# Kernel tuning notes

Hardware: AMD Instinct MI355X
Metric: run time of the kernel (lower is better)

Reference implementation:

```python
import jax, jax.numpy as jnp
import numpy as np

QUERY_DIM = 1024
CONTEXT_DIM = 768
HEADS = 16
DIM_HEAD = 64
INNER = HEADS * DIM_HEAD  # 1024
SCALE = DIM_HEAD ** -0.5


def setup_inputs() -> dict:
    key = jax.random.key(0)
    ks = jax.random.split(key, 8)
    b, nq, nkv = 4, 2048, 1024
    x = jax.random.normal(ks[0], (b, nq, QUERY_DIM), dtype=jnp.float32)
    context = jax.random.normal(ks[1], (b, nkv, CONTEXT_DIM), dtype=jnp.float32)
    mask = jax.random.randint(ks[2], (b, nkv), 0, 2).astype(jnp.bool_)
    s = 0.02
    Wq = jax.random.normal(ks[3], (QUERY_DIM, INNER), dtype=jnp.float32) * s
    Wk = jax.random.normal(ks[4], (CONTEXT_DIM, INNER), dtype=jnp.float32) * s
    Wv = jax.random.normal(ks[5], (CONTEXT_DIM, INNER), dtype=jnp.float32) * s
    Wo = jax.random.normal(ks[6], (INNER, QUERY_DIM), dtype=jnp.float32) * s
    bo = jnp.zeros((QUERY_DIM,), dtype=jnp.float32)
    return {"x": x, "context": context, "mask": mask,
            "Wq": Wq, "Wk": Wk, "Wv": Wv, "Wo": Wo, "bo": bo}


def reference(x, context, mask, Wq, Wk, Wv, Wo, bo):
    b, nq, _ = x.shape
    nkv = context.shape[1]
    h, d = HEADS, DIM_HEAD
    # QKV projections (no bias, as in nn.Linear(..., bias=False))
    q = (x @ Wq).reshape(b, nq, h, d).transpose(0, 2, 1, 3)       # [b,h,i,d]
    k = (context @ Wk).reshape(b, nkv, h, d).transpose(0, 2, 1, 3)  # [b,h,j,d]
    v = (context @ Wv).reshape(b, nkv, h, d).transpose(0, 2, 1, 3)  # [b,h,j,d]
    sim = jnp.einsum('bhid,bhjd->bhij', q, k) * SCALE
    # mask is per-key [b, j]; broadcast over heads and query positions
    neg = jnp.finfo(sim.dtype).min
    sim = jnp.where(mask[:, None, None, :], sim, neg)
    attn = jax.nn.softmax(sim, axis=-1)
    out = jnp.einsum('bhij,bhjd->bhid', attn, v)                  # [b,h,i,d]
    out = out.transpose(0, 2, 1, 3).reshape(b, nq, h * d)          # [b,i,hd]
    return out @ Wo + bo
```

## Files before the change

kernel.cpp:

```cpp
#include <hip/hip_runtime.h>

typedef unsigned short u16;
typedef __attribute__((ext_vector_type(8))) __bf16 bf16x8;
typedef __attribute__((ext_vector_type(4))) float f32x4;
typedef __attribute__((ext_vector_type(4))) u16 u16x4;

#define NB 4
#define NQ 2048
#define NKV 1024
#define NH 16
#define DH 64
#define DIN 1024
#define DCTX 768
#define ATT_SCALE 0.125f
#define NEGBIG -1e30f

__device__ inline u16 f2bf(float f) {
  unsigned u = __builtin_bit_cast(unsigned, f);
  u += 0x7FFFu + ((u >> 16) & 1u);
  return (u16)(u >> 16);
}

__device__ inline unsigned cvtpk(float lo, float hi) {
  unsigned r;
  asm("v_cvt_pk_bf16_f32 %0, %1, %2" : "=v"(r) : "v"(lo), "v"(hi));
  return r;
}

__global__ __launch_bounds__(256) void build_bias(const void* __restrict__ mask,
                                                  float* __restrict__ biasg) {
  __shared__ int notInt, notFloat;
  if (threadIdx.x == 0) { notInt = 0; notFloat = 0; }
  __syncthreads();
  const unsigned* mw = (const unsigned*)mask;
  int bad_i = 0, bad_f = 0;
#pragma unroll
  for (int e = 0; e < 4; e++) {
    unsigned v = mw[threadIdx.x * 4 + e];
    if (v > 1u) bad_i = 1;
    if (v != 0u && v != 0x3f800000u) bad_f = 1;
  }
  if (bad_i) atomicOr(&notInt, 1);
  if (bad_f) atomicOr(&notFloat, 1);
  __syncthreads();
  const int isInt = !notInt, isFloat = !notFloat;
  for (int i = threadIdx.x; i < NB * NKV; i += 256) {
    bool on;
    if (isInt)        on = ((const int*)mask)[i] != 0;
    else if (isFloat) on = ((const float*)mask)[i] != 0.f;
    else              on = ((const unsigned char*)mask)[i] != 0;
    biasg[i] = on ? 0.f : NEGBIG;
  }
}

__global__ __launch_bounds__(256) void cvt_bf16(const float* __restrict__ in,
                                                u16* __restrict__ out, int n) {
  int i = (blockIdx.x * 256 + threadIdx.x) * 4;
  if (i >= n) return;
  float4 v = *(const float4*)(in + i);
  u16x4 o = { f2bf(v.x), f2bf(v.y), f2bf(v.z), f2bf(v.w) };
  *(u16x4*)(out + i) = o;
}

__global__ __launch_bounds__(256) void transpose_cvt(const float* __restrict__ W,
                                                     u16* __restrict__ Wt, int K, int N) {
  __shared__ float tile[32][33];
  int n0 = blockIdx.x * 32, k0 = blockIdx.y * 32;
  int tx = threadIdx.x & 31, ty = threadIdx.x >> 5;
#pragma unroll
  for (int i = 0; i < 32; i += 8)
    tile[ty + i][tx] = W[(size_t)(k0 + ty + i) * N + n0 + tx];
  __syncthreads();
#pragma unroll
  for (int i = 0; i < 32; i += 8)
    Wt[(size_t)(n0 + ty + i) * K + k0 + tx] = f2bf(tile[tx][ty + i]);
}

template<int STORE_BF16>
__global__ __launch_bounds__(256) void gemm_bt(const u16* __restrict__ A,
                                               const u16* __restrict__ Bt,
                                               void* __restrict__ Cout,
                                               const float* __restrict__ bias,
                                               int M, int N, int K) {
  __shared__ __align__(16) u16 As[128 * 32];
  __shared__ __align__(16) u16 Bs[128 * 32];
  const int t = threadIdx.x, w = t >> 6, l = t & 63, g = l >> 4, m16 = l & 15;
  const int brow = blockIdx.y * 128, bcol = blockIdx.x * 128;
  const int wr = w >> 1, wc = w & 1;
  const int r_a = t >> 2;
  const int kb  = (t & 3) * 8;
  f32x4 acc[4][4] = {};

  for (int k0 = 0; k0 < K; k0 += 32) {
#pragma unroll
    for (int i = 0; i < 2; i++) {
      const u16* ga = A + (size_t)(brow + i * 64 + r_a) * K + k0 + kb;
      __builtin_amdgcn_global_load_lds((const __attribute__((address_space(1))) void*)ga,
          (__attribute__((address_space(3))) void*)((char*)As + i * 4096 + w * 1024), 16, 0, 0);
      const u16* gb = Bt + (size_t)(bcol + i * 64 + r_a) * K + k0 + kb;
      __builtin_amdgcn_global_load_lds((const __attribute__((address_space(1))) void*)gb,
          (__attribute__((address_space(3))) void*)((char*)Bs + i * 4096 + w * 1024), 16, 0, 0);
    }
    __syncthreads();
    bf16x8 af[4], bfr[4];
#pragma unroll
    for (int m = 0; m < 4; m++)
      af[m] = *(const bf16x8*)(As + (wr * 64 + m * 16 + m16) * 32 + g * 8);
#pragma unroll
    for (int n = 0; n < 4; n++)
      bfr[n] = *(const bf16x8*)(Bs + (wc * 64 + n * 16 + m16) * 32 + g * 8);
#pragma unroll
    for (int m = 0; m < 4; m++)
#pragma unroll
      for (int n = 0; n < 4; n++)
        acc[m][n] = __builtin_amdgcn_mfma_f32_16x16x32_bf16(af[m], bfr[n], acc[m][n], 0, 0, 0);
    __syncthreads();
  }
#pragma unroll
  for (int m = 0; m < 4; m++) {
    int grow = brow + wr * 64 + m * 16 + g * 4;
#pragma unroll
    for (int n = 0; n < 4; n++) {
      int gcol = bcol + wc * 64 + n * 16 + m16;
#pragma unroll
      for (int r = 0; r < 4; r++) {
        size_t off = (size_t)(grow + r) * N + gcol;
        if (STORE_BF16) ((u16*)Cout)[off] = f2bf(acc[m][n][r]);
        else            ((float*)Cout)[off] = acc[m][n][r] + bias[gcol];
      }
    }
  }
}

__global__ __launch_bounds__(256) void attn(const u16* __restrict__ Q, const u16* __restrict__ Kb,
                                            const u16* __restrict__ Vb,
                                            const float* __restrict__ biasg,
                                            u16* __restrict__ O) {
  const int qt = blockIdx.x, h = blockIdx.y, b = blockIdx.z;
  const int t = threadIdx.x, w = t >> 6, l = t & 63, g = l >> 4, m16 = l & 15;

  __shared__ __align__(16) u16 Kl[64 * 64];
  __shared__ __align__(16) u16 Vt[64 * 64];
  __shared__ __align__(16) unsigned Pl[4][16 * 36];
  __shared__ float biasl[NKV];

  for (int i = t; i < NKV; i += 256) biasl[i] = biasg[(size_t)b * NKV + i];

  const int qrowA = qt * 128 + w * 32 + m16;
  const u16* qpA = Q + (size_t)(b * NQ + qrowA) * DIN + h * DH;
  bf16x8 qA0 = *(const bf16x8*)(qpA + g * 8);
  bf16x8 qA1 = *(const bf16x8*)(qpA + 32 + g * 8);
  const u16* qpB = qpA + 16 * DIN;
  bf16x8 qB0 = *(const bf16x8*)(qpB + g * 8);
  bf16x8 qB1 = *(const bf16x8*)(qpB + 32 + g * 8);

  f32x4 oA[4] = {}, oB[4] = {};
  float lA = 0.f, lB = 0.f;

  for (int j0 = 0; j0 < NKV; j0 += 64) {
#pragma unroll
    for (int n = 0; n < 2; n++) {
      int j = n * 32 + (t >> 3);
      int c = (t & 7) ^ (j & 7);
      const u16* gk = Kb + (size_t)(b * NKV + j0 + j) * DIN + h * DH + c * 8;
      __builtin_amdgcn_global_load_lds((const __attribute__((address_space(1))) void*)gk,
          (__attribute__((address_space(3))) void*)((char*)Kl + n * 4096 + t * 16), 16, 0, 0);
    }
    {
      union { u16 e[16]; int4 q[2]; } vv;
      const u16* gv = Vb + (size_t)(b * NKV + j0 + w * 16) * DIN + h * DH + l;
#pragma unroll
      for (int e = 0; e < 16; e++) vv.e[e] = gv[(size_t)e * DIN];
      int swv = (l ^ (l >> 3)) & 7;
#pragma unroll
      for (int kk = 0; kk < 2; kk++) {
        int cp = (2 * w + kk) ^ swv;
        *(int4*)(Vt + l * 64 + cp * 8) = vv.q[kk];
      }
    }
    __syncthreads();

    f32x4 sA[4], sB[4];
#pragma unroll
    for (int jt = 0; jt < 4; jt++) {
      int jr = jt * 16 + m16;
      const u16* krow = Kl + jr * 64;
      bf16x8 kf0 = *(const bf16x8*)(krow + ((g ^ (jr & 7)) * 8));
      bf16x8 kf1 = *(const bf16x8*)(krow + (((4 + g) ^ (jr & 7)) * 8));
      f32x4 z = {};
      f32x4 t0 = __builtin_amdgcn_mfma_f32_16x16x32_bf16(kf0, qA0, z, 0, 0, 0);
      sA[jt]   = __builtin_amdgcn_mfma_f32_16x16x32_bf16(kf1, qA1, t0, 0, 0, 0);
      f32x4 t1 = __builtin_amdgcn_mfma_f32_16x16x32_bf16(kf0, qB0, z, 0, 0, 0);
      sB[jt]   = __builtin_amdgcn_mfma_f32_16x16x32_bf16(kf1, qB1, t1, 0, 0, 0);
    }
    float4 b4[4];
#pragma unroll
    for (int jt = 0; jt < 4; jt++) b4[jt] = *(const float4*)&biasl[j0 + jt * 16 + g * 4];

    unsigned* plw = &Pl[w][0];
    {
#pragma unroll
      for (int jt = 0; jt < 4; jt++) {
        float p0 = __expf(fmaf(sA[jt][0], ATT_SCALE, b4[jt].x));
        float p1 = __expf(fmaf(sA[jt][1], ATT_SCALE, b4[jt].y));
        float p2 = __expf(fmaf(sA[jt][2], ATT_SCALE, b4[jt].z));
        float p3 = __expf(fmaf(sA[jt][3], ATT_SCALE, b4[jt].w));
        lA += (p0 + p1) + (p2 + p3);
        uint2 u; u.x = cvtpk(p0, p1); u.y = cvtpk(p2, p3);
        *(uint2*)&plw[m16 * 36 + jt * 8 + 2 * g] = u;
      }
      asm volatile("" ::: "memory");
      bf16x8 pf0 = *(const bf16x8*)&plw[m16 * 36 + 4 * g];
      bf16x8 pf1 = *(const bf16x8*)&plw[m16 * 36 + 16 + 4 * g];
#pragma unroll
      for (int dt = 0; dt < 4; dt++) {
        int d = dt * 16 + m16;
        int swd = (d ^ (d >> 3)) & 7;
        const u16* vrow = Vt + d * 64;
        bf16x8 vf0 = *(const bf16x8*)(vrow + ((g ^ swd) * 8));
        bf16x8 vf1 = *(const bf16x8*)(vrow + (((4 + g) ^ swd) * 8));
        oA[dt] = __builtin_amdgcn_mfma_f32_16x16x32_bf16(pf0, vf0, oA[dt], 0, 0, 0);
        oA[dt] = __builtin_amdgcn_mfma_f32_16x16x32_bf16(pf1, vf1, oA[dt], 0, 0, 0);
      }
    }
    asm volatile("" ::: "memory");
    {
#pragma unroll
      for (int jt = 0; jt < 4; jt++) {
        float p0 = __expf(fmaf(sB[jt][0], ATT_SCALE, b4[jt].x));
        float p1 = __expf(fmaf(sB[jt][1], ATT_SCALE, b4[jt].y));
        float p2 = __expf(fmaf(sB[jt][2], ATT_SCALE, b4[jt].z));
        float p3 = __expf(fmaf(sB[jt][3], ATT_SCALE, b4[jt].w));
        lB += (p0 + p1) + (p2 + p3);
        uint2 u; u.x = cvtpk(p0, p1); u.y = cvtpk(p2, p3);
        *(uint2*)&plw[m16 * 36 + jt * 8 + 2 * g] = u;
      }
      asm volatile("" ::: "memory");
      bf16x8 pf0 = *(const bf16x8*)&plw[m16 * 36 + 4 * g];
      bf16x8 pf1 = *(const bf16x8*)&plw[m16 * 36 + 16 + 4 * g];
#pragma unroll
      for (int dt = 0; dt < 4; dt++) {
        int d = dt * 16 + m16;
        int swd = (d ^ (d >> 3)) & 7;
        const u16* vrow = Vt + d * 64;
        bf16x8 vf0 = *(const bf16x8*)(vrow + ((g ^ swd) * 8));
        bf16x8 vf1 = *(const bf16x8*)(vrow + (((4 + g) ^ swd) * 8));
        oB[dt] = __builtin_amdgcn_mfma_f32_16x16x32_bf16(pf0, vf0, oB[dt], 0, 0, 0);
        oB[dt] = __builtin_amdgcn_mfma_f32_16x16x32_bf16(pf1, vf1, oB[dt], 0, 0, 0);
      }
    }
    __syncthreads();
  }

  lA += __shfl_xor(lA, 16); lA += __shfl_xor(lA, 32);
  lB += __shfl_xor(lB, 16); lB += __shfl_xor(lB, 32);
  float invA[4], invB[4];
#pragma unroll
  for (int r = 0; r < 4; r++) {
    invA[r] = 1.f / __shfl(lA, g * 4 + r);
    invB[r] = 1.f / __shfl(lB, g * 4 + r);
  }
  u16* opA = O + (size_t)(b * NQ + qt * 128 + w * 32) * DIN + h * DH;
  u16* opB = opA + 16 * DIN;
#pragma unroll
  for (int dt = 0; dt < 4; dt++)
#pragma unroll
    for (int r = 0; r < 4; r++) {
      opA[(size_t)(g * 4 + r) * DIN + dt * 16 + m16] = f2bf(oA[dt][r] * invA[r]);
      opB[(size_t)(g * 4 + r) * DIN + dt * 16 + m16] = f2bf(oB[dt][r] * invB[r]);
    }
}

extern "C" void kernel_launch(void* const* d_in, const int* in_sizes, int n_in,
                              void* d_out, int out_size, void* d_ws, size_t ws_size,
                              hipStream_t stream) {
  const float* x   = (const float*)d_in[0];
  const float* ctx = (const float*)d_in[1];
  const void*  mask = (const void*)d_in[2];
  const float* Wq  = (const float*)d_in[3];
  const float* Wk  = (const float*)d_in[4];
  const float* Wv  = (const float*)d_in[5];
  const float* Wo  = (const float*)d_in[6];
  const float* bo  = (const float*)d_in[7];
  float* out = (float*)d_out;

  char* ws = (char*)d_ws;
  u16* xb  = (u16*)(ws);
  u16* cb  = (u16*)(ws + 16777216);
  u16* wqt = (u16*)(ws + 23068672);
  u16* wkt = (u16*)(ws + 25165824);
  u16* wvt = (u16*)(ws + 26738688);
  u16* wot = (u16*)(ws + 28311552);
  u16* qb  = (u16*)(ws + 30408704);
  u16* kb  = (u16*)(ws + 47185920);
  u16* vb  = (u16*)(ws + 55574528);
  float* biasg = (float*)(ws + 63963136);
  u16* ab  = xb;

  build_bias<<<1, 256, 0, stream>>>(mask, biasg);
  cvt_bf16<<<8192, 256, 0, stream>>>(x, xb, 8388608);
  cvt_bf16<<<3072, 256, 0, stream>>>(ctx, cb, 3145728);
  transpose_cvt<<<dim3(32, 32), 256, 0, stream>>>(Wq, wqt, 1024, 1024);
  transpose_cvt<<<dim3(32, 24), 256, 0, stream>>>(Wk, wkt, 768, 1024);
  transpose_cvt<<<dim3(32, 24), 256, 0, stream>>>(Wv, wvt, 768, 1024);
  transpose_cvt<<<dim3(32, 32), 256, 0, stream>>>(Wo, wot, 1024, 1024);

  gemm_bt<1><<<dim3(8, 64), 256, 0, stream>>>(xb, wqt, qb, nullptr, 8192, 1024, 1024);
  gemm_bt<1><<<dim3(8, 32), 256, 0, stream>>>(cb, wkt, kb, nullptr, 4096, 1024, 768);
  gemm_bt<1><<<dim3(8, 32), 256, 0, stream>>>(cb, wvt, vb, nullptr, 4096, 1024, 768);

  attn<<<dim3(16, 16, 4), 256, 0, stream>>>(qb, kb, vb, biasg, ab);

  gemm_bt<0><<<dim3(8, 64), 256, 0, stream>>>(ab, wot, out, bo, 8192, 1024, 1024);
}
```

Measured before the change: 302.1 us.

## Double-buffer GEMM and attention tiles, fuse K/V projection, fold scale into Q

The GEMM and attention kernels now keep two LDS buffers each, so the next tile's global loads overlap the MFMA work on the current tile and one of the two barriers per iteration goes away. The K and V projections are merged into a single GEMM with N=2048 that writes an interleaved KV buffer, which attention reads with stride 2048. The softmax scale times log2(e) is folded into the Q projection epilogue, so attention can use the raw v_exp_f32 (exp2) with no per-element multiply. This costs twice the LDS per block and a wider K/V read stride. It also assumes the mask bias is in log2 units, which works here only because it is 0 or a very large negative value.

```diff
diff --git a/kernel.cpp b/kernel.cpp
--- a/kernel.cpp
+++ b/kernel.cpp
@@ -12,8 +12,8 @@
 #define DH 64
 #define DIN 1024
 #define DCTX 768
-#define ATT_SCALE 0.125f
 #define NEGBIG -1e30f
+#define QSC 0.180336881f
 
 __device__ inline u16 f2bf(float f) {
   unsigned u = __builtin_bit_cast(unsigned, f);
@@ -24,6 +24,12 @@
 __device__ inline unsigned cvtpk(float lo, float hi) {
   unsigned r;
   asm("v_cvt_pk_bf16_f32 %0, %1, %2" : "=v"(r) : "v"(lo), "v"(hi));
+  return r;
+}
+
+__device__ inline float exp2a(float x) {
+  float r;
+  asm("v_exp_f32 %0, %1" : "=v"(r) : "v"(x));
   return r;
 }
 
@@ -76,46 +82,64 @@
     Wt[(size_t)(n0 + ty + i) * K + k0 + tx] = f2bf(tile[tx][ty + i]);
 }
 
-template<int STORE_BF16>
+template<int STORE_MODE>
 __global__ __launch_bounds__(256) void gemm_bt(const u16* __restrict__ A,
                                                const u16* __restrict__ Bt,
                                                void* __restrict__ Cout,
                                                const float* __restrict__ bias,
                                                int M, int N, int K) {
-  __shared__ __align__(16) u16 As[128 * 32];
-  __shared__ __align__(16) u16 Bs[128 * 32];
+  __shared__ __align__(16) u16 As[2][128 * 32];
+  __shared__ __align__(16) u16 Bs[2][128 * 32];
   const int t = threadIdx.x, w = t >> 6, l = t & 63, g = l >> 4, m16 = l & 15;
   const int brow = blockIdx.y * 128, bcol = blockIdx.x * 128;
   const int wr = w >> 1, wc = w & 1;
   const int r_a = t >> 2;
   const int kb  = (t & 3) * 8;
+  const int nk = K >> 5;
   f32x4 acc[4][4] = {};
 
-  for (int k0 = 0; k0 < K; k0 += 32) {
-#pragma unroll
-    for (int i = 0; i < 2; i++) {
-      const u16* ga = A + (size_t)(brow + i * 64 + r_a) * K + k0 + kb;
-      __builtin_amdgcn_global_load_lds((const __attribute__((address_space(1))) void*)ga,
-          (__attribute__((address_space(3))) void*)((char*)As + i * 4096 + w * 1024), 16, 0, 0);
-      const u16* gb = Bt + (size_t)(bcol + i * 64 + r_a) * K + k0 + kb;
-      __builtin_amdgcn_global_load_lds((const __attribute__((address_space(1))) void*)gb,
-          (__attribute__((address_space(3))) void*)((char*)Bs + i * 4096 + w * 1024), 16, 0, 0);
-    }
-    __syncthreads();
+#define G_STAGE(ks, bsel)                                                              \
+  {                                                                                    \
+    int k0_ = (ks) << 5;                                                               \
+    _Pragma("unroll")                                                                  \
+    for (int i = 0; i < 2; i++) {                                                      \
+      const u16* ga = A + (size_t)(brow + i * 64 + r_a) * K + k0_ + kb;                \
+      __builtin_amdgcn_global_load_lds(                                                \
+          (const __attribute__((address_space(1))) void*)ga,                           \
+          (__attribute__((address_space(3))) void*)((char*)As + (bsel) * 8192 + i * 4096 + w * 1024), \
+          16, 0, 0);                                                                   \
+      const u16* gb = Bt + (size_t)(bcol + i * 64 + r_a) * K + k0_ + kb;               \
+      __builtin_amdgcn_global_load_lds(                                                \
+          (const __attribute__((address_space(1))) void*)gb,                           \
+          (__attribute__((address_space(3))) void*)((char*)Bs + (bsel) * 8192 + i * 4096 + w * 1024), \
+          16, 0, 0);                                                                   \
+    }                                                                                  \
+  }
+
+  G_STAGE(0, 0);
+  asm volatile("s_waitcnt vmcnt(0)" ::: "memory");
+  __builtin_amdgcn_s_barrier();
+
+  for (int ks = 0; ks < nk; ++ks) {
+    const int cur = ks & 1;
     bf16x8 af[4], bfr[4];
 #pragma unroll
     for (int m = 0; m < 4; m++)
-      af[m] = *(const bf16x8*)(As + (wr * 64 + m * 16 + m16) * 32 + g * 8);
+      af[m] = *(const bf16x8*)(&As[cur][(wr * 64 + m * 16 + m16) * 32 + g * 8]);
 #pragma unroll
     for (int n = 0; n < 4; n++)
-      bfr[n] = *(const bf16x8*)(Bs + (wc * 64 + n * 16 + m16) * 32 + g * 8);
+      bfr[n] = *(const bf16x8*)(&Bs[cur][(wc * 64 + n * 16 + m16) * 32 + g * 8]);
+    if (ks + 1 < nk) G_STAGE(ks + 1, cur ^ 1);
 #pragma unroll
     for (int m = 0; m < 4; m++)
 #pragma unroll
       for (int n = 0; n < 4; n++)
         acc[m][n] = __builtin_amdgcn_mfma_f32_16x16x32_bf16(af[m], bfr[n], acc[m][n], 0, 0, 0);
-    __syncthreads();
-  }
+    asm volatile("s_waitcnt vmcnt(0)" ::: "memory");
+    __builtin_amdgcn_s_barrier();
+  }
+#undef G_STAGE
+
 #pragma unroll
   for (int m = 0; m < 4; m++) {
     int grow = brow + wr * 64 + m * 16 + g * 4;
@@ -125,8 +149,9 @@
 #pragma unroll
       for (int r = 0; r < 4; r++) {
         size_t off = (size_t)(grow + r) * N + gcol;
-        if (STORE_BF16) ((u16*)Cout)[off] = f2bf(acc[m][n][r]);
-        else            ((float*)Cout)[off] = acc[m][n][r] + bias[gcol];
+        if (STORE_MODE == 0)      ((float*)Cout)[off] = acc[m][n][r] + bias[gcol];
+        else if (STORE_MODE == 1) ((u16*)Cout)[off] = f2bf(acc[m][n][r]);
+        else                      ((u16*)Cout)[off] = f2bf(acc[m][n][r] * QSC);
       }
     }
   }
@@ -135,12 +160,12 @@
 __global__ __launch_bounds__(256) void attn(const u16* __restrict__ Q, const u16* __restrict__ Kb,
                                             const u16* __restrict__ Vb,
                                             const float* __restrict__ biasg,
-                                            u16* __restrict__ O) {
+                                            u16* __restrict__ O, int kvs) {
   const int qt = blockIdx.x, h = blockIdx.y, b = blockIdx.z;
   const int t = threadIdx.x, w = t >> 6, l = t & 63, g = l >> 4, m16 = l & 15;
 
-  __shared__ __align__(16) u16 Kl[64 * 64];
-  __shared__ __align__(16) u16 Vt[64 * 64];
+  __shared__ __align__(16) u16 Kl[2][64 * 64];
+  __shared__ __align__(16) u16 Vt[2][64 * 64];
   __shared__ __align__(16) unsigned Pl[4][16 * 36];
   __shared__ float biasl[NKV];
 
@@ -157,34 +182,58 @@
   f32x4 oA[4] = {}, oB[4] = {};
   float lA = 0.f, lB = 0.f;
 
-  for (int j0 = 0; j0 < NKV; j0 += 64) {
-#pragma unroll
-    for (int n = 0; n < 2; n++) {
-      int j = n * 32 + (t >> 3);
-      int c = (t & 7) ^ (j & 7);
-      const u16* gk = Kb + (size_t)(b * NKV + j0 + j) * DIN + h * DH + c * 8;
-      __builtin_amdgcn_global_load_lds((const __attribute__((address_space(1))) void*)gk,
-          (__attribute__((address_space(3))) void*)((char*)Kl + n * 4096 + t * 16), 16, 0, 0);
-    }
-    {
-      union { u16 e[16]; int4 q[2]; } vv;
-      const u16* gv = Vb + (size_t)(b * NKV + j0 + w * 16) * DIN + h * DH + l;
-#pragma unroll
-      for (int e = 0; e < 16; e++) vv.e[e] = gv[(size_t)e * DIN];
-      int swv = (l ^ (l >> 3)) & 7;
-#pragma unroll
-      for (int kk = 0; kk < 2; kk++) {
-        int cp = (2 * w + kk) ^ swv;
-        *(int4*)(Vt + l * 64 + cp * 8) = vv.q[kk];
-      }
-    }
-    __syncthreads();
+  union VV { u16 e[16]; int4 q[2]; };
+  VV vv;
+  const int swv = (l ^ (l >> 3)) & 7;
+
+#define GATHER_V(j0)                                                          \
+  {                                                                           \
+    const u16* gv = Vb + (size_t)(b * NKV + (j0) + w * 16) * kvs + h * DH + l; \
+    _Pragma("unroll")                                                         \
+    for (int e = 0; e < 16; e++) vv.e[e] = gv[(size_t)e * kvs];               \
+  }
+#define STAGE_K(j0, bsel)                                                     \
+  {                                                                           \
+    _Pragma("unroll")                                                         \
+    for (int n = 0; n < 2; n++) {                                             \
+      int j_ = n * 32 + (t >> 3);                                             \
+      int c_ = (t & 7) ^ (j_ & 7);                                            \
+      const u16* gk = Kb + (size_t)(b * NKV + (j0) + j_) * kvs + h * DH + c_ * 8; \
+      __builtin_amdgcn_global_load_lds(                                       \
+          (const __attribute__((address_space(1))) void*)gk,                  \
+          (__attribute__((address_space(3))) void*)((char*)Kl + (bsel) * 8192 + n * 4096 + t * 16), \
+          16, 0, 0);                                                          \
+    }                                                                         \
+  }
+#define WRITE_V(bsel)                                                         \
+  {                                                                           \
+    _Pragma("unroll")                                                         \
+    for (int kk = 0; kk < 2; kk++) {                                          \
+      int cp = (2 * w + kk) ^ swv;                                            \
+      *(int4*)(&Vt[bsel][l * 64 + cp * 8]) = vv.q[kk];                        \
+    }                                                                         \
+  }
+
+  GATHER_V(0);
+  STAGE_K(0, 0);
+  asm volatile("s_waitcnt vmcnt(0)" ::: "memory");
+  WRITE_V(0);
+  asm volatile("s_waitcnt lgkmcnt(0)" ::: "memory");
+  __builtin_amdgcn_s_barrier();
+
+  for (int it = 0; it < 16; ++it) {
+    const int cur = it & 1, nxt = cur ^ 1;
+    const int j0 = it * 64;
+    if (it + 1 < 16) {
+      GATHER_V(j0 + 64);
+      STAGE_K(j0 + 64, nxt);
+    }
 
     f32x4 sA[4], sB[4];
 #pragma unroll
     for (int jt = 0; jt < 4; jt++) {
       int jr = jt * 16 + m16;
-      const u16* krow = Kl + jr * 64;
+      const u16* krow = &Kl[cur][jr * 64];
       bf16x8 kf0 = *(const bf16x8*)(krow + ((g ^ (jr & 7)) * 8));
       bf16x8 kf1 = *(const bf16x8*)(krow + (((4 + g) ^ (jr & 7)) * 8));
       f32x4 z = {};
@@ -201,10 +250,10 @@
     {
 #pragma unroll
       for (int jt = 0; jt < 4; jt++) {
-        float p0 = __expf(fmaf(sA[jt][0], ATT_SCALE, b4[jt].x));
-        float p1 = __expf(fmaf(sA[jt][1], ATT_SCALE, b4[jt].y));
-        float p2 = __expf(fmaf(sA[jt][2], ATT_SCALE, b4[jt].z));
-        float p3 = __expf(fmaf(sA[jt][3], ATT_SCALE, b4[jt].w));
+        float p0 = exp2a(sA[jt][0] + b4[jt].x);
+        float p1 = exp2a(sA[jt][1] + b4[jt].y);
+        float p2 = exp2a(sA[jt][2] + b4[jt].z);
+        float p3 = exp2a(sA[jt][3] + b4[jt].w);
         lA += (p0 + p1) + (p2 + p3);
         uint2 u; u.x = cvtpk(p0, p1); u.y = cvtpk(p2, p3);
         *(uint2*)&plw[m16 * 36 + jt * 8 + 2 * g] = u;
@@ -216,7 +265,7 @@
       for (int dt = 0; dt < 4; dt++) {
         int d = dt * 16 + m16;
         int swd = (d ^ (d >> 3)) & 7;
-        const u16* vrow = Vt + d * 64;
+        const u16* vrow = &Vt[cur][d * 64];
         bf16x8 vf0 = *(const bf16x8*)(vrow + ((g ^ swd) * 8));
         bf16x8 vf1 = *(const bf16x8*)(vrow + (((4 + g) ^ swd) * 8));
         oA[dt] = __builtin_amdgcn_mfma_f32_16x16x32_bf16(pf0, vf0, oA[dt], 0, 0, 0);
@@ -227,10 +276,10 @@
     {
 #pragma unroll
       for (int jt = 0; jt < 4; jt++) {
-        float p0 = __expf(fmaf(sB[jt][0], ATT_SCALE, b4[jt].x));
-        float p1 = __expf(fmaf(sB[jt][1], ATT_SCALE, b4[jt].y));
-        float p2 = __expf(fmaf(sB[jt][2], ATT_SCALE, b4[jt].z));
-        float p3 = __expf(fmaf(sB[jt][3], ATT_SCALE, b4[jt].w));
+        float p0 = exp2a(sB[jt][0] + b4[jt].x);
+        float p1 = exp2a(sB[jt][1] + b4[jt].y);
+        float p2 = exp2a(sB[jt][2] + b4[jt].z);
+        float p3 = exp2a(sB[jt][3] + b4[jt].w);
         lB += (p0 + p1) + (p2 + p3);
         uint2 u; u.x = cvtpk(p0, p1); u.y = cvtpk(p2, p3);
         *(uint2*)&plw[m16 * 36 + jt * 8 + 2 * g] = u;
@@ -242,15 +291,21 @@
       for (int dt = 0; dt < 4; dt++) {
         int d = dt * 16 + m16;
         int swd = (d ^ (d >> 3)) & 7;
-        const u16* vrow = Vt + d * 64;
+        const u16* vrow = &Vt[cur][d * 64];
         bf16x8 vf0 = *(const bf16x8*)(vrow + ((g ^ swd) * 8));
         bf16x8 vf1 = *(const bf16x8*)(vrow + (((4 + g) ^ swd) * 8));
         oB[dt] = __builtin_amdgcn_mfma_f32_16x16x32_bf16(pf0, vf0, oB[dt], 0, 0, 0);
         oB[dt] = __builtin_amdgcn_mfma_f32_16x16x32_bf16(pf1, vf1, oB[dt], 0, 0, 0);
       }
     }
-    __syncthreads();
-  }
+    asm volatile("s_waitcnt vmcnt(0)" ::: "memory");
+    if (it + 1 < 16) WRITE_V(nxt);
+    asm volatile("s_waitcnt lgkmcnt(0)" ::: "memory");
+    __builtin_amdgcn_s_barrier();
+  }
+#undef GATHER_V
+#undef STAGE_K
+#undef WRITE_V
 
   lA += __shfl_xor(lA, 16); lA += __shfl_xor(lA, 32);
   lB += __shfl_xor(lB, 16); lB += __shfl_xor(lB, 32);
@@ -285,31 +340,28 @@
   float* out = (float*)d_out;
 
   char* ws = (char*)d_ws;
-  u16* xb  = (u16*)(ws);
-  u16* cb  = (u16*)(ws + 16777216);
-  u16* wqt = (u16*)(ws + 23068672);
-  u16* wkt = (u16*)(ws + 25165824);
-  u16* wvt = (u16*)(ws + 26738688);
-  u16* wot = (u16*)(ws + 28311552);
-  u16* qb  = (u16*)(ws + 30408704);
-  u16* kb  = (u16*)(ws + 47185920);
-  u16* vb  = (u16*)(ws + 55574528);
+  u16* xb   = (u16*)(ws);
+  u16* cb   = (u16*)(ws + 16777216);
+  u16* wqt  = (u16*)(ws + 23068672);
+  u16* wkv  = (u16*)(ws + 25165824);
+  u16* wot  = (u16*)(ws + 28311552);
+  u16* qb   = (u16*)(ws + 30408704);
+  u16* kvb  = (u16*)(ws + 47185920);
   float* biasg = (float*)(ws + 63963136);
-  u16* ab  = xb;
+  u16* ab   = xb;
 
   build_bias<<<1, 256, 0, stream>>>(mask, biasg);
   cvt_bf16<<<8192, 256, 0, stream>>>(x, xb, 8388608);
   cvt_bf16<<<3072, 256, 0, stream>>>(ctx, cb, 3145728);
   transpose_cvt<<<dim3(32, 32), 256, 0, stream>>>(Wq, wqt, 1024, 1024);
-  transpose_cvt<<<dim3(32, 24), 256, 0, stream>>>(Wk, wkt, 768, 1024);
-  transpose_cvt<<<dim3(32, 24), 256, 0, stream>>>(Wv, wvt, 768, 1024);
+  transpose_cvt<<<dim3(32, 24), 256, 0, stream>>>(Wk, wkv, 768, 1024);
+  transpose_cvt<<<dim3(32, 24), 256, 0, stream>>>(Wv, wkv + 1024 * 768, 768, 1024);
   transpose_cvt<<<dim3(32, 32), 256, 0, stream>>>(Wo, wot, 1024, 1024);
 
-  gemm_bt<1><<<dim3(8, 64), 256, 0, stream>>>(xb, wqt, qb, nullptr, 8192, 1024, 1024);
-  gemm_bt<1><<<dim3(8, 32), 256, 0, stream>>>(cb, wkt, kb, nullptr, 4096, 1024, 768);
-  gemm_bt<1><<<dim3(8, 32), 256, 0, stream>>>(cb, wvt, vb, nullptr, 4096, 1024, 768);
-
-  attn<<<dim3(16, 16, 4), 256, 0, stream>>>(qb, kb, vb, biasg, ab);
+  gemm_bt<2><<<dim3(8, 64), 256, 0, stream>>>(xb, wqt, qb, nullptr, 8192, 1024, 1024);
+  gemm_bt<1><<<dim3(16, 32), 256, 0, stream>>>(cb, wkv, kvb, nullptr, 4096, 2048, 768);
+
+  attn<<<dim3(16, 16, 4), 256, 0, stream>>>(qb, kvb, kvb + 1024, biasg, ab, 2048);
 
   gemm_bt<0><<<dim3(8, 64), 256, 0, stream>>>(ab, wot, out, bo, 8192, 1024, 1024);
 }
```

Result: faster. 275.0 us (-9.0%).
